# Kernel optimization log

Hardware: AMD Instinct MI355X
Metric: run time of the kernel (lower is better)

Reference implementation:

```python
import jax, jax.numpy as jnp
import numpy as np

N = 100000   # nodes
E = 1600000  # edges
F_IN = 256   # input features
H = 128      # hidden
C = 40       # classes


def setup_inputs() -> dict:
    key = jax.random.key(0)
    ks = jax.random.split(key, 6)
    x = jax.random.normal(ks[0], (N, F_IN), dtype=jnp.float32)
    edge_index = jax.random.randint(ks[1], (2, E), 0, N, dtype=jnp.int32)
    edge_attr = jax.random.uniform(ks[2], (E,), dtype=jnp.float32)
    # Glorot-style init like GCNConv
    W1 = jax.random.normal(ks[3], (F_IN, H), dtype=jnp.float32) * (1.0 / np.sqrt(F_IN))
    b1 = jnp.zeros((H,), dtype=jnp.float32)
    W2 = jax.random.normal(ks[4], (H, C), dtype=jnp.float32) * (1.0 / np.sqrt(H))
    b2 = jnp.zeros((C,), dtype=jnp.float32)
    return {"x": x, "edge_index": edge_index, "edge_attr": edge_attr,
            "W1": W1, "b1": b1, "W2": W2, "b2": b2}


def _gcn_norm(edge_index, edge_weight, num_nodes):
    # PyG gcn_norm: add self-loops (weight 1), symmetric D^{-1/2} A D^{-1/2}
    row, col = edge_index[0], edge_index[1]
    loop = jnp.arange(num_nodes, dtype=row.dtype)
    row = jnp.concatenate([row, loop])
    col = jnp.concatenate([col, loop])
    ew = jnp.concatenate([edge_weight, jnp.ones((num_nodes,), edge_weight.dtype)])
    deg = jax.ops.segment_sum(ew, col, num_segments=num_nodes)
    dinv = jnp.where(deg > 0, jax.lax.rsqrt(deg), 0.0)
    norm = dinv[row] * ew * dinv[col]
    return row, col, norm


def _gcn_conv(x, row, col, norm, W, b):
    h = x @ W                              # [N, out] dense transform first
    msg = h[row] * norm[:, None]           # gather source + edge scaling
    out = jax.ops.segment_sum(msg, col, num_segments=x.shape[0])  # scatter-add
    return out + b


def reference(x, edge_index, edge_attr, W1, b1, W2, b2):
    row, col, norm = _gcn_norm(edge_index, edge_attr, x.shape[0])
    h = _gcn_conv(x, row, col, norm, W1, b1)
    h = jax.nn.relu(h)
    # dropout is identity in eval mode
    h = _gcn_conv(h, row, col, norm, W2, b2)
    return jax.nn.log_softmax(h, axis=1)
```

## Files before the change

### kernel.cpp

```cpp
#include <hip/hip_runtime.h>

#define N_NODES 100000
#define N_EDGES 1600000
#define F_INPUT 256
#define H_DIM   128
#define C_DIM   40
#define NBKT    391
#define NCHK    1563
#define NSC1    391
#define NGEMM1  1563
#define NPREB   152

typedef short  bf8   __attribute__((ext_vector_type(8)));
typedef float  f32x4 __attribute__((ext_vector_type(4)));
typedef float  f32x2 __attribute__((ext_vector_type(2)));
typedef unsigned short u16x8 __attribute__((ext_vector_type(8)));

static __device__ __forceinline__ unsigned short f2bf(float f) {
    union { float f; unsigned u; } v; v.f = f;
    unsigned r = v.u + 0x7FFFu + ((v.u >> 16) & 1u);
    return (unsigned short)(r >> 16);
}
static __device__ __forceinline__ f32x2 bfpair(unsigned u) {
    union { unsigned u; float f; } lo, hi;
    lo.u = u << 16; hi.u = u & 0xFFFF0000u;
    return (f32x2){lo.f, hi.f};
}

__global__ void k_preh(const float* __restrict__ W1, const float* __restrict__ W2,
                       unsigned short* Wp1, unsigned short* Wp2,
                       const int* __restrict__ col, unsigned* __restrict__ histG) {
    int tid = threadIdx.x;
    if (blockIdx.x >= NPREB) {
        __shared__ unsigned histL[NBKT];
        int chunk = blockIdx.x - NPREB;
        for (int i = tid; i < NBKT; i += 256) histL[i] = 0;
        __syncthreads();
        int e0 = chunk * 1024 + tid;
#pragma unroll
        for (int k = 0; k < 4; k++) {
            int e = e0 + k * 256;
            if (e < N_EDGES) atomicAdd(&histL[col[e] >> 8], 1u);
        }
        __syncthreads();
        for (int i = tid; i < NBKT; i += 256) histG[(size_t)i * NCHK + chunk] = histL[i];
        return;
    }
    int idx = blockIdx.x * 256 + tid;
    if (idx < 32768) {
        int j = idx & 7, lane = (idx >> 3) & 63, ks = (idx >> 9) & 7, nt = idx >> 12;
        int m = lane & 15, q = lane >> 4;
        Wp1[idx] = f2bf(W1[(ks * 32 + q * 8 + j) * H_DIM + nt * 16 + m]);
    }
    int idx2 = idx - 32768;
    if (idx2 >= 0 && idx2 < 6144) {
        int j = idx2 & 7, lane = (idx2 >> 3) & 63, ks = (idx2 >> 9) & 3, nt = idx2 >> 11;
        int m = lane & 15, q = lane >> 4;
        int n = nt * 16 + m;
        Wp2[idx2] = (n < C_DIM) ? f2bf(W2[(ks * 32 + q * 8 + j) * C_DIM + n]) : (unsigned short)0;
    }
}

__global__ void k_scanB(unsigned* histG, unsigned* bktTotal) {
    __shared__ unsigned s[256];
    int B = blockIdx.x, t = threadIdx.x;
    unsigned carry = 0;
    for (int c0 = 0; c0 < NCHK; c0 += 256) {
        int idx = c0 + t;
        unsigned v = (idx < NCHK) ? histG[(size_t)B * NCHK + idx] : 0;
        s[t] = v; __syncthreads();
        for (int off = 1; off < 256; off <<= 1) {
            unsigned u = (t >= off) ? s[t - off] : 0;
            __syncthreads();
            s[t] += u;
            __syncthreads();
        }
        if (idx < NCHK) histG[(size_t)B * NCHK + idx] = s[t] - v + carry;
        unsigned tot = s[255];
        __syncthreads();
        carry += tot;
    }
    if (t == 0) bktTotal[B] = carry;
}

__global__ void k_scanC(const unsigned* __restrict__ bktTotal, unsigned* bucketBase) {
    __shared__ unsigned s[256];
    int t = threadIdx.x;
    unsigned carry = 0;
    for (int c0 = 0; c0 < NBKT; c0 += 256) {
        int idx = c0 + t;
        unsigned v = (idx < NBKT) ? bktTotal[idx] : 0;
        s[t] = v; __syncthreads();
        for (int off = 1; off < 256; off <<= 1) {
            unsigned u = (t >= off) ? s[t - off] : 0;
            __syncthreads();
            s[t] += u;
            __syncthreads();
        }
        if (idx < NBKT) bucketBase[idx] = s[t] - v + carry;
        unsigned tot = s[255];
        __syncthreads();
        carry += tot;
    }
    if (t == 0) bucketBase[NBKT] = carry;
}

__global__ void k_scat1(const int* __restrict__ row, const int* __restrict__ col,
                        const float* __restrict__ ea,
                        const unsigned* __restrict__ histG,
                        const unsigned* __restrict__ bucketBase,
                        int2* __restrict__ recs) {
    __shared__ unsigned base_l[NBKT];
    __shared__ unsigned cursor[NBKT];
    int blk = blockIdx.x, t = threadIdx.x;
    for (int i = t; i < NBKT; i += 512) {
        base_l[i] = bucketBase[i] + histG[(size_t)i * NCHK + blk * 4];
        cursor[i] = 0;
    }
    __syncthreads();
    int e0 = blk * 4096 + t;
#pragma unroll
    for (int k = 0; k < 8; k++) {
        int e = e0 + k * 512;
        if (e < N_EDGES) {
            int c = col[e];
            int bkt = c >> 8;
            unsigned r = atomicAdd(&cursor[bkt], 1u);
            int pos = (int)(base_l[bkt] + r);
            recs[pos] = make_int2((row[e] << 8) | (c & 255), __float_as_int(ea[e]));
        }
    }
}

__global__ void k_pass2(const int2* __restrict__ recs,
                        const unsigned* __restrict__ bucketBase,
                        int* __restrict__ start, int* __restrict__ cnt,
                        float* __restrict__ dinv, int2* __restrict__ csr) {
    __shared__ unsigned cntL[256];
    __shared__ unsigned wsL[256];
    __shared__ unsigned s[256];
    __shared__ int startL[256];
    __shared__ unsigned cur[256];
    int B = blockIdx.x, t = threadIdx.x;
    if (t < 256) { cntL[t] = 0; wsL[t] = 0; cur[t] = 0; }
    __syncthreads();
    int lo = (int)bucketBase[B], hi = (int)bucketBase[B + 1];
    for (int i = lo + t; i < hi; i += 512) {
        int2 rc = recs[i];
        int cl = rc.x & 255;
        atomicAdd(&cntL[cl], 1u);
        unsigned q = __float2uint_rn(__int_as_float(rc.y) * 65536.0f);
        atomicAdd(&wsL[cl], q);
    }
    __syncthreads();
    unsigned v = 0;
    if (t < 256) { v = cntL[t]; s[t] = v; }
    __syncthreads();
    for (int off = 1; off < 256; off <<= 1) {
        unsigned u = 0;
        if (t < 256 && t >= (unsigned)off) u = s[t - off];
        __syncthreads();
        if (t < 256) s[t] += u;
        __syncthreads();
    }
    if (t < 256) {
        int st = lo + (int)(s[t] - v);
        startL[t] = st;
        int node = B * 256 + t;
        if (node < N_NODES) {
            start[node] = st;
            cnt[node] = (int)v;
            dinv[node] = rsqrtf((float)(65536u + wsL[t]) * (1.0f / 65536.0f));
        }
    }
    __syncthreads();
    for (int i = lo + t; i < hi; i += 512) {
        int2 rc = recs[i];
        int cl = rc.x & 255;
        int rw = rc.x >> 8;
        unsigned r = atomicAdd(&cur[cl], 1u);
        csr[startL[cl] + (int)r] = make_int2(rw, rc.y);
    }
}

__global__ __launch_bounds__(256, 2) void k_gemm1(
        const float* __restrict__ x, const unsigned short* __restrict__ Wp,
        const float* __restrict__ dinv, unsigned short* __restrict__ h) {
    __shared__ unsigned short sWp[32768];
    __shared__ unsigned short lds_out[64 * H_DIM];
    int tid = threadIdx.x;
    int wave = tid >> 6, lane = tid & 63;
    int m = lane & 15, q = lane >> 4;
    int tile = blockIdx.x;
    int row0 = tile * 64 + wave * 16;
    int rowA = row0 + m; if (rowA >= N_NODES) rowA = N_NODES - 1;
    const float* xr = x + (long)rowA * F_INPUT + q * 8;

    float4 xv[16];
#pragma unroll
    for (int ks = 0; ks < 8; ks++) {
        xv[2 * ks]     = *(const float4*)(xr + ks * 32);
        xv[2 * ks + 1] = *(const float4*)(xr + ks * 32 + 4);
    }
#pragma unroll
    for (int it = 0; it < 16; it++) {
        int idx = (it * 256 + tid) * 8;
        *(u16x8*)(sWp + idx) = *(const u16x8*)(Wp + idx);
    }
    __syncthreads();

    f32x4 acc[8];
#pragma unroll
    for (int i = 0; i < 8; i++) acc[i] = (f32x4){0.f, 0.f, 0.f, 0.f};
#pragma unroll
    for (int ks = 0; ks < 8; ks++) {
        float4 a0 = xv[2 * ks], a1 = xv[2 * ks + 1];
        bf8 a;
        a[0] = (short)f2bf(a0.x); a[1] = (short)f2bf(a0.y);
        a[2] = (short)f2bf(a0.z); a[3] = (short)f2bf(a0.w);
        a[4] = (short)f2bf(a1.x); a[5] = (short)f2bf(a1.y);
        a[6] = (short)f2bf(a1.z); a[7] = (short)f2bf(a1.w);
#pragma unroll
        for (int nt = 0; nt < 8; nt++) {
            bf8 bb = *(const bf8*)(sWp + (((nt * 8 + ks) * 64 + lane) << 3));
            acc[nt] = __builtin_amdgcn_mfma_f32_16x16x32_bf16(a, bb, acc[nt], 0, 0, 0);
        }
    }
    int lrow = wave * 16 + q * 4;
    float dv[4];
#pragma unroll
    for (int r = 0; r < 4; r++) {
        int gr = tile * 64 + lrow + r; if (gr >= N_NODES) gr = N_NODES - 1;
        dv[r] = dinv[gr];
    }
#pragma unroll
    for (int nt = 0; nt < 8; nt++)
#pragma unroll
        for (int r = 0; r < 4; r++)
            lds_out[(lrow + r) * H_DIM + nt * 16 + m] = f2bf(acc[nt][r] * dv[r]);
    __syncthreads();
    int valid = N_NODES - tile * 64; if (valid > 64) valid = 64;
    unsigned short* gbase = h + (size_t)tile * 64 * H_DIM;
#pragma unroll
    for (int i = 0; i < 4; i++) {
        int idx = (i * 256 + tid) * 8;
        if (idx < valid * H_DIM)
            *(u16x8*)(gbase + idx) = *(const u16x8*)(lds_out + idx);
    }
}

__global__ __launch_bounds__(256) void k_agg1(
        const unsigned* __restrict__ hw, const int2* __restrict__ csr,
        const int* __restrict__ start, const int* __restrict__ cnt,
        const float* __restrict__ dinv, const float* __restrict__ b1,
        unsigned* __restrict__ h1w) {
    int c = blockIdx.x * 4 + (threadIdx.x >> 6);
    int lane = threadIdx.x & 63;
    if (c >= N_NODES) return;
    float di = dinv[c];
    int su = __builtin_amdgcn_readfirstlane(start[c]);
    int n  = __builtin_amdgcn_readfirstlane(cnt[c]);
    f32x2 acc = bfpair(hw[(size_t)c * 64 + lane]);
    int i = 0;
    for (; i + 4 <= n; i += 4) {
        int2 p0 = csr[su + i], p1 = csr[su + i + 1];
        int2 p2 = csr[su + i + 2], p3 = csr[su + i + 3];
        int r0 = __builtin_amdgcn_readfirstlane(p0.x);
        int r1 = __builtin_amdgcn_readfirstlane(p1.x);
        int r2 = __builtin_amdgcn_readfirstlane(p2.x);
        int r3 = __builtin_amdgcn_readfirstlane(p3.x);
        float w0 = __int_as_float(__builtin_amdgcn_readfirstlane(p0.y));
        float w1 = __int_as_float(__builtin_amdgcn_readfirstlane(p1.y));
        float w2 = __int_as_float(__builtin_amdgcn_readfirstlane(p2.y));
        float w3 = __int_as_float(__builtin_amdgcn_readfirstlane(p3.y));
        unsigned a0 = hw[(size_t)r0 * 64 + lane];
        unsigned a1 = hw[(size_t)r1 * 64 + lane];
        unsigned a2 = hw[(size_t)r2 * 64 + lane];
        unsigned a3 = hw[(size_t)r3 * 64 + lane];
        acc += (f32x2){w0, w0} * bfpair(a0);
        acc += (f32x2){w1, w1} * bfpair(a1);
        acc += (f32x2){w2, w2} * bfpair(a2);
        acc += (f32x2){w3, w3} * bfpair(a3);
    }
    for (; i < n; i++) {
        int2 p = csr[su + i];
        int r = __builtin_amdgcn_readfirstlane(p.x);
        float w = __int_as_float(__builtin_amdgcn_readfirstlane(p.y));
        unsigned a = hw[(size_t)r * 64 + lane];
        acc += (f32x2){w, w} * bfpair(a);
    }
    float2 bb = ((const float2*)b1)[lane];
    float o0 = fmaxf(di * acc.x + bb.x, 0.f);
    float o1 = fmaxf(di * acc.y + bb.y, 0.f);
    h1w[(size_t)c * 64 + lane] = (unsigned)f2bf(o0) | ((unsigned)f2bf(o1) << 16);
}

__global__ __launch_bounds__(256, 4) void k_gemm2(const unsigned short* __restrict__ h1,
                        const unsigned short* __restrict__ Wp,
                        const float* __restrict__ dinv,
                        unsigned short* __restrict__ h2) {
    __shared__ unsigned short lds_out[64 * C_DIM];
    int tid = threadIdx.x;
    int wave = tid >> 6, lane = tid & 63;
    int m = lane & 15, q = lane >> 4;
    int row0 = blockIdx.x * 64 + wave * 16;
    int rowA = row0 + m; if (rowA >= N_NODES) rowA = N_NODES - 1;

    f32x4 acc[3];
#pragma unroll
    for (int i = 0; i < 3; i++) acc[i] = (f32x4){0.f, 0.f, 0.f, 0.f};
    const unsigned short* hr = h1 + (long)rowA * H_DIM + q * 8;
#pragma unroll
    for (int ks = 0; ks < 4; ks++) {
        bf8 a = *(const bf8*)(hr + ks * 32);
#pragma unroll
        for (int nt = 0; nt < 3; nt++) {
            bf8 b = *(const bf8*)(Wp + (((nt * 4 + ks) * 64 + lane) << 3));
            acc[nt] = __builtin_amdgcn_mfma_f32_16x16x32_bf16(a, b, acc[nt], 0, 0, 0);
        }
    }
    int lrow = wave * 16 + q * 4;
    float dv[4];
#pragma unroll
    for (int r = 0; r < 4; r++) {
        int gr = blockIdx.x * 64 + lrow + r; if (gr >= N_NODES) gr = N_NODES - 1;
        dv[r] = dinv[gr];
    }
#pragma unroll
    for (int nt = 0; nt < 3; nt++)
#pragma unroll
        for (int r = 0; r < 4; r++) {
            int colo = nt * 16 + m;
            if (colo < C_DIM)
                lds_out[(lrow + r) * C_DIM + colo] = f2bf(acc[nt][r] * dv[r]);
        }
    __syncthreads();
    int valid = N_NODES - blockIdx.x * 64; if (valid > 64) valid = 64;
    unsigned short* gbase = h2 + (size_t)blockIdx.x * 64 * 64;
    int total10 = valid * 10;
    for (int i = tid; i < total10; i += 256) {
        int rw = i / 10, part = i - rw * 10;
        *(uint2*)(gbase + rw * 64 + part * 4) = *(const uint2*)(lds_out + rw * C_DIM + part * 4);
    }
}

__global__ void k_agg2(const unsigned short* __restrict__ h2, const int2* __restrict__ csr,
                       const int* __restrict__ start, const int* __restrict__ cnt,
                       const float* __restrict__ dinv, const float* __restrict__ b2,
                       float* __restrict__ out) {
    int c = (blockIdx.x * blockDim.x + threadIdx.x) >> 6;
    int lane = threadIdx.x & 63;
    if (c >= N_NODES) return;
    int eg = lane >> 3, cl = lane & 7;
    float di = dinv[c];
    int s = start[c];
    int n = cnt[c];

    float w[3]; int r[3];
#pragma unroll
    for (int t = 0; t < 3; t++) {
        int i = eg + 8 * t;
        int2 p = csr[s + ((i < n) ? i : 0)];
        bool val = (i < n);
        r[t] = val ? p.x : c;
        w[t] = val ? __int_as_float(p.y) : 0.f;
    }
    uint4 gv[3] = {{0,0,0,0},{0,0,0,0},{0,0,0,0}};
    uint4 selfv = {0, 0, 0, 0};
    if (cl < 5) {
#pragma unroll
        for (int t = 0; t < 3; t++)
            gv[t] = *(const uint4*)(h2 + (long)r[t] * 64 + cl * 8);
        if (eg == 0) selfv = *(const uint4*)(h2 + (long)c * 64 + cl * 8);
    }
    f32x2 acc[4];
#pragma unroll
    for (int k = 0; k < 4; k++) acc[k] = (f32x2){0.f, 0.f};
    {
        unsigned sv[4] = {selfv.x, selfv.y, selfv.z, selfv.w};
        if (eg == 0 && cl < 5)
#pragma unroll
            for (int k = 0; k < 4; k++) acc[k] += bfpair(sv[k]);
    }
#pragma unroll
    for (int t = 0; t < 3; t++) {
        unsigned vv[4] = {gv[t].x, gv[t].y, gv[t].z, gv[t].w};
        f32x2 ww = (f32x2){w[t], w[t]};
#pragma unroll
        for (int k = 0; k < 4; k++) acc[k] += ww * bfpair(vv[k]);
    }
    for (int i = 24 + eg; i < n; i += 8) {
        int2 p = csr[s + i];
        if (cl < 5) {
            uint4 v4 = *(const uint4*)(h2 + (long)p.x * 64 + cl * 8);
            unsigned vv[4] = {v4.x, v4.y, v4.z, v4.w};
            float wt = __int_as_float(p.y);
            f32x2 ww = (f32x2){wt, wt};
#pragma unroll
            for (int k = 0; k < 4; k++) acc[k] += ww * bfpair(vv[k]);
        }
    }
#pragma unroll
    for (int k = 0; k < 4; k++) {
        acc[k].x += __shfl_xor(acc[k].x, 8);  acc[k].y += __shfl_xor(acc[k].y, 8);
        acc[k].x += __shfl_xor(acc[k].x, 16); acc[k].y += __shfl_xor(acc[k].y, 16);
        acc[k].x += __shfl_xor(acc[k].x, 32); acc[k].y += __shfl_xor(acc[k].y, 32);
    }
    float v[8];
    float lm = -INFINITY;
    if (cl < 5) {
#pragma unroll
        for (int k = 0; k < 4; k++) {
            v[2 * k]     = di * acc[k].x + b2[cl * 8 + 2 * k];
            v[2 * k + 1] = di * acc[k].y + b2[cl * 8 + 2 * k + 1];
            lm = fmaxf(lm, fmaxf(v[2 * k], v[2 * k + 1]));
        }
    }
    lm = fmaxf(lm, __shfl_xor(lm, 1));
    lm = fmaxf(lm, __shfl_xor(lm, 2));
    lm = fmaxf(lm, __shfl_xor(lm, 4));
    float ls = 0.f;
    if (cl < 5) {
#pragma unroll
        for (int j = 0; j < 8; j++) ls += __expf(v[j] - lm);
    }
    ls += __shfl_xor(ls, 1);
    ls += __shfl_xor(ls, 2);
    ls += __shfl_xor(ls, 4);
    if (eg == 0 && cl < 5) {
        float lsm = lm + logf(ls);
        f32x4 o0, o1;
#pragma unroll
        for (int j = 0; j < 4; j++) { o0[j] = v[j] - lsm; o1[j] = v[j + 4] - lsm; }
        *(f32x4*)(out + (long)c * C_DIM + cl * 8)     = o0;
        *(f32x4*)(out + (long)c * C_DIM + cl * 8 + 4) = o1;
    }
}

extern "C" void kernel_launch(void* const* d_in, const int* in_sizes, int n_in,
                              void* d_out, int out_size, void* d_ws, size_t ws_size,
                              hipStream_t stream) {
    const float* x  = (const float*)d_in[0];
    const int*   ei = (const int*)d_in[1];
    const float* ea = (const float*)d_in[2];
    const float* W1 = (const float*)d_in[3];
    const float* b1 = (const float*)d_in[4];
    const float* W2 = (const float*)d_in[5];
    const float* b2 = (const float*)d_in[6];
    const int* row = ei;
    const int* col = ei + N_EDGES;

    char* ws = (char*)d_ws;
    size_t off = 0;
    auto alloc = [&](size_t bytes) -> void* {
        void* p = ws + off;
        off = (off + bytes + 255) & ~(size_t)255;
        return p;
    };
    unsigned*       histG   = (unsigned*)alloc((size_t)NBKT * NCHK * 4);
    unsigned*       bktTot  = (unsigned*)alloc((size_t)NBKT * 4);
    unsigned*       bktBase = (unsigned*)alloc((size_t)(NBKT + 1) * 4);
    int*            start   = (int*)alloc((size_t)N_NODES * 4);
    int*            cnt     = (int*)alloc((size_t)N_NODES * 4);
    float*          dinv    = (float*)alloc((size_t)N_NODES * 4);
    int2*           recs    = (int2*)alloc((size_t)N_EDGES * 8);
    int2*           csr     = (int2*)alloc((size_t)(N_EDGES + 8) * 8);
    unsigned short* Wp1     = (unsigned short*)alloc(32768 * 2);
    unsigned short* Wp2     = (unsigned short*)alloc(6144 * 2);
    unsigned short* h       = (unsigned short*)alloc((size_t)(N_NODES + 64) * H_DIM * 2);
    unsigned short* h1      = (unsigned short*)alloc((size_t)N_NODES * H_DIM * 2);
    unsigned short* h2      = (unsigned short*)alloc((size_t)(N_NODES + 64) * 64 * 2);

    k_preh<<<NPREB + NCHK, 256, 0, stream>>>(W1, W2, Wp1, Wp2, col, histG);
    k_scanB<<<NBKT, 256, 0, stream>>>(histG, bktTot);
    k_scanC<<<1, 256, 0, stream>>>(bktTot, bktBase);
    k_scat1<<<NSC1, 512, 0, stream>>>(row, col, ea, histG, bktBase, recs);
    k_pass2<<<NBKT, 512, 0, stream>>>(recs, bktBase, start, cnt, dinv, csr);
    k_gemm1<<<NGEMM1, 256, 0, stream>>>(x, Wp1, dinv, h);
    k_agg1<<<N_NODES / 4, 256, 0, stream>>>((const unsigned*)h, csr, start, cnt, dinv, b1,
                                            (unsigned*)h1);
    k_gemm2<<<(N_NODES + 63) / 64, 256, 0, stream>>>(h1, Wp2, dinv, h2);
    k_agg2<<<N_NODES / 4, 256, 0, stream>>>(h2, csr, start, cnt, dinv, b2, (float*)d_out);
}
```

Before: 362.5 us.

## Interleave GEMM1 tiles into histogram, scatter and pass2 kernels; fold source dinv into CSR weights

Removes the standalone GEMM1 kernel and splits its tiles across the histogram, scatter and degree-count kernels. Every third block in those kernels runs a 2-tile GEMM role, so the dense transform overlaps the sort and scan stages. Because GEMM1 no longer depends on dinv, the source-side D^-1/2 is moved into the CSR edge weights in a new pass2b kernel, and the self-loop term in the aggregations is scaled by dinv explicitly. The cost is a 96KB shared-memory footprint at one block per CU for the mixed kernels, a larger histogram chunk size, and one extra kernel launch.

```diff
diff --git a/kernel.cpp b/kernel.cpp
--- a/kernel.cpp
+++ b/kernel.cpp
@@ -6,10 +6,11 @@
 #define H_DIM   128
 #define C_DIM   40
 #define NBKT    391
-#define NCHK    1563
-#define NSC1    391
+#define NCHK    782
 #define NGEMM1  1563
-#define NPREB   152
+#define NMEGA   1173
+#define NSCAT   587
+#define NP2A    587
 
 typedef short  bf8   __attribute__((ext_vector_type(8)));
 typedef float  f32x4 __attribute__((ext_vector_type(4)));
@@ -27,26 +28,9 @@
     return (f32x2){lo.f, hi.f};
 }
 
-__global__ void k_preh(const float* __restrict__ W1, const float* __restrict__ W2,
-                       unsigned short* Wp1, unsigned short* Wp2,
-                       const int* __restrict__ col, unsigned* __restrict__ histG) {
-    int tid = threadIdx.x;
-    if (blockIdx.x >= NPREB) {
-        __shared__ unsigned histL[NBKT];
-        int chunk = blockIdx.x - NPREB;
-        for (int i = tid; i < NBKT; i += 256) histL[i] = 0;
-        __syncthreads();
-        int e0 = chunk * 1024 + tid;
-#pragma unroll
-        for (int k = 0; k < 4; k++) {
-            int e = e0 + k * 256;
-            if (e < N_EDGES) atomicAdd(&histL[col[e] >> 8], 1u);
-        }
-        __syncthreads();
-        for (int i = tid; i < NBKT; i += 256) histG[(size_t)i * NCHK + chunk] = histL[i];
-        return;
-    }
-    int idx = blockIdx.x * 256 + tid;
+__global__ void k_pre(const float* __restrict__ W1, const float* __restrict__ W2,
+                      unsigned short* Wp1, unsigned short* Wp2) {
+    int idx = blockIdx.x * 256 + threadIdx.x;
     if (idx < 32768) {
         int j = idx & 7, lane = (idx >> 3) & 63, ks = (idx >> 9) & 7, nt = idx >> 12;
         int m = lane & 15, q = lane >> 4;
@@ -59,6 +43,89 @@
         int n = nt * 16 + m;
         Wp2[idx2] = (n < C_DIM) ? f2bf(W2[(ks * 32 + q * 8 + j) * C_DIM + n]) : (unsigned short)0;
     }
+}
+
+static __device__ __forceinline__ void gemm_role(
+        int tileBase, int tid, char* smem,
+        const float* __restrict__ x, const unsigned short* __restrict__ Wp,
+        unsigned short* __restrict__ h) {
+    unsigned short* sWp = (unsigned short*)smem;
+    unsigned short* lds_out = (unsigned short*)(smem + 65536);
+    int sub = tid >> 8;
+    int t256 = tid & 255;
+    int wave = t256 >> 6, lane = t256 & 63;
+    int m = lane & 15, q = lane >> 4;
+    int tile = tileBase + sub; if (tile >= NGEMM1) tile = NGEMM1 - 1;
+    int rowA = tile * 64 + wave * 16 + m; if (rowA >= N_NODES) rowA = N_NODES - 1;
+    const float* xr = x + (long)rowA * F_INPUT + q * 8;
+
+    float4 xv[16];
+#pragma unroll
+    for (int ks = 0; ks < 8; ks++) {
+        xv[2 * ks]     = *(const float4*)(xr + ks * 32);
+        xv[2 * ks + 1] = *(const float4*)(xr + ks * 32 + 4);
+    }
+#pragma unroll
+    for (int it = 0; it < 8; it++) {
+        int idx = (it * 512 + tid) * 8;
+        *(u16x8*)(sWp + idx) = *(const u16x8*)(Wp + idx);
+    }
+    __syncthreads();
+
+    f32x4 acc[8];
+#pragma unroll
+    for (int i = 0; i < 8; i++) acc[i] = (f32x4){0.f, 0.f, 0.f, 0.f};
+#pragma unroll
+    for (int ks = 0; ks < 8; ks++) {
+        float4 a0 = xv[2 * ks], a1 = xv[2 * ks + 1];
+        bf8 a;
+        a[0] = (short)f2bf(a0.x); a[1] = (short)f2bf(a0.y);
+        a[2] = (short)f2bf(a0.z); a[3] = (short)f2bf(a0.w);
+        a[4] = (short)f2bf(a1.x); a[5] = (short)f2bf(a1.y);
+        a[6] = (short)f2bf(a1.z); a[7] = (short)f2bf(a1.w);
+#pragma unroll
+        for (int nt = 0; nt < 8; nt++) {
+            bf8 bb = *(const bf8*)(sWp + (((nt * 8 + ks) * 64 + lane) << 3));
+            acc[nt] = __builtin_amdgcn_mfma_f32_16x16x32_bf16(a, bb, acc[nt], 0, 0, 0);
+        }
+    }
+    unsigned short* ldsT = lds_out + sub * (64 * H_DIM);
+    int lrow = wave * 16 + q * 4;
+#pragma unroll
+    for (int nt = 0; nt < 8; nt++)
+#pragma unroll
+        for (int r = 0; r < 4; r++)
+            ldsT[(lrow + r) * H_DIM + nt * 16 + m] = f2bf(acc[nt][r]);
+    __syncthreads();
+    int valid = N_NODES - tile * 64; if (valid > 64) valid = 64;
+    unsigned short* gbase = h + (size_t)tile * 64 * H_DIM;
+#pragma unroll
+    for (int i = 0; i < 4; i++) {
+        int idx = (i * 256 + t256) * 8;
+        if (idx < valid * H_DIM)
+            *(u16x8*)(gbase + idx) = *(const u16x8*)(ldsT + idx);
+    }
+}
+
+__global__ __launch_bounds__(512, 1) void k_mega(
+        const float* __restrict__ x, const unsigned short* __restrict__ Wp,
+        unsigned short* __restrict__ h,
+        const int* __restrict__ col, unsigned* __restrict__ histG) {
+    __shared__ __align__(16) char smem[98304];
+    int b = blockIdx.x, t = threadIdx.x;
+    if (b % 3 == 0) { gemm_role(2 * (b / 3), t, smem, x, Wp, h); return; }
+    unsigned* histL = (unsigned*)smem;
+    int chunk = b - b / 3 - 1;
+    for (int i = t; i < NBKT; i += 512) histL[i] = 0;
+    __syncthreads();
+    int e0 = chunk * 2048 + t;
+#pragma unroll
+    for (int k = 0; k < 4; k++) {
+        int e = e0 + k * 512;
+        if (e < N_EDGES) atomicAdd(&histL[col[e] >> 8], 1u);
+    }
+    __syncthreads();
+    for (int i = t; i < NBKT; i += 512) histG[(size_t)i * NCHK + chunk] = histL[i];
 }
 
 __global__ void k_scanB(unsigned* histG, unsigned* bktTotal) {
@@ -105,16 +172,22 @@
     if (t == 0) bucketBase[NBKT] = carry;
 }
 
-__global__ void k_scat1(const int* __restrict__ row, const int* __restrict__ col,
-                        const float* __restrict__ ea,
-                        const unsigned* __restrict__ histG,
-                        const unsigned* __restrict__ bucketBase,
-                        int2* __restrict__ recs) {
-    __shared__ unsigned base_l[NBKT];
-    __shared__ unsigned cursor[NBKT];
-    int blk = blockIdx.x, t = threadIdx.x;
+__global__ __launch_bounds__(512, 1) void k_scat1(
+        const int* __restrict__ row, const int* __restrict__ col,
+        const float* __restrict__ ea,
+        const unsigned* __restrict__ histG,
+        const unsigned* __restrict__ bucketBase,
+        int2* __restrict__ recs,
+        const float* __restrict__ x, const unsigned short* __restrict__ Wp,
+        unsigned short* __restrict__ h) {
+    __shared__ __align__(16) char smem[98304];
+    int b = blockIdx.x, t = threadIdx.x;
+    if (b % 3 == 0) { gemm_role(782 + 2 * (b / 3), t, smem, x, Wp, h); return; }
+    unsigned* base_l = (unsigned*)smem;
+    unsigned* cursor = base_l + NBKT;
+    int blk = b - b / 3 - 1;
     for (int i = t; i < NBKT; i += 512) {
-        base_l[i] = bucketBase[i] + histG[(size_t)i * NCHK + blk * 4];
+        base_l[i] = bucketBase[i] + histG[(size_t)i * NCHK + blk * 2];
         cursor[i] = 0;
     }
     __syncthreads();
@@ -132,17 +205,20 @@
     }
 }
 
-__global__ void k_pass2(const int2* __restrict__ recs,
-                        const unsigned* __restrict__ bucketBase,
-                        int* __restrict__ start, int* __restrict__ cnt,
-                        float* __restrict__ dinv, int2* __restrict__ csr) {
-    __shared__ unsigned cntL[256];
-    __shared__ unsigned wsL[256];
-    __shared__ unsigned s[256];
-    __shared__ int startL[256];
-    __shared__ unsigned cur[256];
-    int B = blockIdx.x, t = threadIdx.x;
-    if (t < 256) { cntL[t] = 0; wsL[t] = 0; cur[t] = 0; }
+__global__ __launch_bounds__(512, 1) void k_pass2a(
+        const int2* __restrict__ recs,
+        const unsigned* __restrict__ bucketBase,
+        int* __restrict__ start, int* __restrict__ cnt, float* __restrict__ dinv,
+        const float* __restrict__ x, const unsigned short* __restrict__ Wp,
+        unsigned short* __restrict__ h) {
+    __shared__ __align__(16) char smem[98304];
+    int b = blockIdx.x, t = threadIdx.x;
+    if (b % 3 == 0) { gemm_role(1174 + 2 * (b / 3), t, smem, x, Wp, h); return; }
+    unsigned* cntL = (unsigned*)smem;
+    unsigned* wsL  = cntL + 256;
+    unsigned* s    = wsL + 256;
+    int B = b - b / 3 - 1;
+    if (t < 256) { cntL[t] = 0; wsL[t] = 0; }
     __syncthreads();
     int lo = (int)bucketBase[B], hi = (int)bucketBase[B + 1];
     for (int i = lo + t; i < hi; i += 512) {
@@ -164,88 +240,37 @@
         __syncthreads();
     }
     if (t < 256) {
-        int st = lo + (int)(s[t] - v);
-        startL[t] = st;
         int node = B * 256 + t;
         if (node < N_NODES) {
-            start[node] = st;
+            start[node] = lo + (int)(s[t] - v);
             cnt[node] = (int)v;
             dinv[node] = rsqrtf((float)(65536u + wsL[t]) * (1.0f / 65536.0f));
         }
     }
-    __syncthreads();
+}
+
+__global__ void k_pass2b(const int2* __restrict__ recs,
+                         const unsigned* __restrict__ bucketBase,
+                         const int* __restrict__ start,
+                         const float* __restrict__ dinv,
+                         int2* __restrict__ csr) {
+    __shared__ int startL[256];
+    __shared__ unsigned cur[256];
+    int B = blockIdx.x, t = threadIdx.x;
+    if (t < 256) {
+        int node = B * 256 + t;
+        startL[t] = (node < N_NODES) ? start[node] : 0;
+        cur[t] = 0;
+    }
+    __syncthreads();
+    int lo = (int)bucketBase[B], hi = (int)bucketBase[B + 1];
     for (int i = lo + t; i < hi; i += 512) {
         int2 rc = recs[i];
         int cl = rc.x & 255;
         int rw = rc.x >> 8;
+        float w = __int_as_float(rc.y) * dinv[rw];
         unsigned r = atomicAdd(&cur[cl], 1u);
-        csr[startL[cl] + (int)r] = make_int2(rw, rc.y);
-    }
-}
-
-__global__ __launch_bounds__(256, 2) void k_gemm1(
-        const float* __restrict__ x, const unsigned short* __restrict__ Wp,
-        const float* __restrict__ dinv, unsigned short* __restrict__ h) {
-    __shared__ unsigned short sWp[32768];
-    __shared__ unsigned short lds_out[64 * H_DIM];
-    int tid = threadIdx.x;
-    int wave = tid >> 6, lane = tid & 63;
-    int m = lane & 15, q = lane >> 4;
-    int tile = blockIdx.x;
-    int row0 = tile * 64 + wave * 16;
-    int rowA = row0 + m; if (rowA >= N_NODES) rowA = N_NODES - 1;
-    const float* xr = x + (long)rowA * F_INPUT + q * 8;
-
-    float4 xv[16];
-#pragma unroll
-    for (int ks = 0; ks < 8; ks++) {
-        xv[2 * ks]     = *(const float4*)(xr + ks * 32);
-        xv[2 * ks + 1] = *(const float4*)(xr + ks * 32 + 4);
-    }
-#pragma unroll
-    for (int it = 0; it < 16; it++) {
-        int idx = (it * 256 + tid) * 8;
-        *(u16x8*)(sWp + idx) = *(const u16x8*)(Wp + idx);
-    }
-    __syncthreads();
-
-    f32x4 acc[8];
-#pragma unroll
-    for (int i = 0; i < 8; i++) acc[i] = (f32x4){0.f, 0.f, 0.f, 0.f};
-#pragma unroll
-    for (int ks = 0; ks < 8; ks++) {
-        float4 a0 = xv[2 * ks], a1 = xv[2 * ks + 1];
-        bf8 a;
-        a[0] = (short)f2bf(a0.x); a[1] = (short)f2bf(a0.y);
-        a[2] = (short)f2bf(a0.z); a[3] = (short)f2bf(a0.w);
-        a[4] = (short)f2bf(a1.x); a[5] = (short)f2bf(a1.y);
-        a[6] = (short)f2bf(a1.z); a[7] = (short)f2bf(a1.w);
-#pragma unroll
-        for (int nt = 0; nt < 8; nt++) {
-            bf8 bb = *(const bf8*)(sWp + (((nt * 8 + ks) * 64 + lane) << 3));
-            acc[nt] = __builtin_amdgcn_mfma_f32_16x16x32_bf16(a, bb, acc[nt], 0, 0, 0);
-        }
-    }
-    int lrow = wave * 16 + q * 4;
-    float dv[4];
-#pragma unroll
-    for (int r = 0; r < 4; r++) {
-        int gr = tile * 64 + lrow + r; if (gr >= N_NODES) gr = N_NODES - 1;
-        dv[r] = dinv[gr];
-    }
-#pragma unroll
-    for (int nt = 0; nt < 8; nt++)
-#pragma unroll
-        for (int r = 0; r < 4; r++)
-            lds_out[(lrow + r) * H_DIM + nt * 16 + m] = f2bf(acc[nt][r] * dv[r]);
-    __syncthreads();
-    int valid = N_NODES - tile * 64; if (valid > 64) valid = 64;
-    unsigned short* gbase = h + (size_t)tile * 64 * H_DIM;
-#pragma unroll
-    for (int i = 0; i < 4; i++) {
-        int idx = (i * 256 + tid) * 8;
-        if (idx < valid * H_DIM)
-            *(u16x8*)(gbase + idx) = *(const u16x8*)(lds_out + idx);
+        csr[startL[cl] + (int)r] = make_int2(rw, __float_as_int(w));
     }
 }
 
@@ -260,7 +285,11 @@
     float di = dinv[c];
     int su = __builtin_amdgcn_readfirstlane(start[c]);
     int n  = __builtin_amdgcn_readfirstlane(cnt[c]);
-    f32x2 acc = bfpair(hw[(size_t)c * 64 + lane]);
+    f32x2 acc;
+    {
+        f32x2 sp = bfpair(hw[(size_t)c * 64 + lane]);
+        acc = (f32x2){di, di} * sp;
+    }
     int i = 0;
     for (; i + 4 <= n; i += 4) {
         int2 p0 = csr[su + i], p1 = csr[su + i + 1];
@@ -297,7 +326,6 @@
 
 __global__ __launch_bounds__(256, 4) void k_gemm2(const unsigned short* __restrict__ h1,
                         const unsigned short* __restrict__ Wp,
-                        const float* __restrict__ dinv,
                         unsigned short* __restrict__ h2) {
     __shared__ unsigned short lds_out[64 * C_DIM];
     int tid = threadIdx.x;
@@ -320,19 +348,13 @@
         }
     }
     int lrow = wave * 16 + q * 4;
-    float dv[4];
-#pragma unroll
-    for (int r = 0; r < 4; r++) {
-        int gr = blockIdx.x * 64 + lrow + r; if (gr >= N_NODES) gr = N_NODES - 1;
-        dv[r] = dinv[gr];
-    }
 #pragma unroll
     for (int nt = 0; nt < 3; nt++)
 #pragma unroll
         for (int r = 0; r < 4; r++) {
             int colo = nt * 16 + m;
             if (colo < C_DIM)
-                lds_out[(lrow + r) * C_DIM + colo] = f2bf(acc[nt][r] * dv[r]);
+                lds_out[(lrow + r) * C_DIM + colo] = f2bf(acc[nt][r]);
         }
     __syncthreads();
     int valid = N_NODES - blockIdx.x * 64; if (valid > 64) valid = 64;
@@ -378,9 +400,10 @@
     for (int k = 0; k < 4; k++) acc[k] = (f32x2){0.f, 0.f};
     {
         unsigned sv[4] = {selfv.x, selfv.y, selfv.z, selfv.w};
+        f32x2 dd = (f32x2){di, di};
         if (eg == 0 && cl < 5)
 #pragma unroll
-            for (int k = 0; k < 4; k++) acc[k] += bfpair(sv[k]);
+            for (int k = 0; k < 4; k++) acc[k] += dd * bfpair(sv[k]);
     }
 #pragma unroll
     for (int t = 0; t < 3; t++) {
@@ -471,14 +494,15 @@
     unsigned short* h1      = (unsigned short*)alloc((size_t)N_NODES * H_DIM * 2);
     unsigned short* h2      = (unsigned short*)alloc((size_t)(N_NODES + 64) * 64 * 2);
 
-    k_preh<<<NPREB + NCHK, 256, 0, stream>>>(W1, W2, Wp1, Wp2, col, histG);
+    k_pre<<<152, 256, 0, stream>>>(W1, W2, Wp1, Wp2);
+    k_mega<<<NMEGA, 512, 0, stream>>>(x, Wp1, h, col, histG);
     k_scanB<<<NBKT, 256, 0, stream>>>(histG, bktTot);
     k_scanC<<<1, 256, 0, stream>>>(bktTot, bktBase);
-    k_scat1<<<NSC1, 512, 0, stream>>>(row, col, ea, histG, bktBase, recs);
-    k_pass2<<<NBKT, 512, 0, stream>>>(recs, bktBase, start, cnt, dinv, csr);
-    k_gemm1<<<NGEMM1, 256, 0, stream>>>(x, Wp1, dinv, h);
+    k_scat1<<<NSCAT, 512, 0, stream>>>(row, col, ea, histG, bktBase, recs, x, Wp1, h);
+    k_pass2a<<<NP2A, 512, 0, stream>>>(recs, bktBase, start, cnt, dinv, x, Wp1, h);
+    k_pass2b<<<NBKT, 512, 0, stream>>>(recs, bktBase, start, dinv, csr);
     k_agg1<<<N_NODES / 4, 256, 0, stream>>>((const unsigned*)h, csr, start, cnt, dinv, b1,
                                             (unsigned*)h1);
-    k_gemm2<<<(N_NODES + 63) / 64, 256, 0, stream>>>(h1, Wp2, dinv, h2);
+    k_gemm2<<<(N_NODES + 63) / 64, 256, 0, stream>>>(h1, Wp2, h2);
     k_agg2<<<N_NODES / 4, 256, 0, stream>>>(h2, csr, start, cnt, dinv, b2, (float*)d_out);
 }
```

After: 370.4 us. 2.2% more time.
